# Optimization experiments

Measured on AMD Instinct MI355X. Metric: run time of the kernel, lower is better.

## Reference

```python
import jax, jax.numpy as jnp
import numpy as np

B, L, D_IN, H, TAGS = 16, 128, 512, 256, 45


def setup_inputs() -> dict:
    key = jax.random.key(0)
    ks = jax.random.split(key, 10)
    s = 0.02
    return {
        "contextualized": jax.random.normal(ks[0], (B, L, D_IN), jnp.float32),
        "sentence_lengths": jax.random.randint(ks[1], (B,), 64, L + 1, jnp.int32),
        "desired_arcs": jax.random.randint(ks[2], (B, L), 0, L + 1, jnp.int32),
        "desired_labels": jax.random.randint(ks[3], (B, L), 0, TAGS, jnp.int32),
        "W1": jax.random.normal(ks[4], (D_IN, H), jnp.float32) * s,
        "b1": jnp.zeros((H,), jnp.float32),
        "root": jax.random.normal(ks[5], (H,), jnp.float32) * s,
        "Wp": jax.random.normal(ks[6], (2 * H, H), jnp.float32) * s,
        "bp": jnp.zeros((H,), jnp.float32),
        "W_arc": jax.random.normal(ks[7], (H, 1), jnp.float32) * s,
        "b_arc": jnp.zeros((1,), jnp.float32),
        "W_lab": jax.random.normal(ks[8], (H, TAGS), jnp.float32) * s,
        "b_lab": jnp.zeros((TAGS,), jnp.float32),
    }


def _forward(contextualized, sentence_lengths, desired_arcs, desired_labels,
             W1, b1, root, Wp, bp, W_arc, b_arc, W_lab, b_lab):
    b, l, _ = contextualized.shape
    h = W1.shape[1]
    # token representations: dense + relu
    hidden = jax.nn.relu(contextualized @ W1 + b1)                      # [B,L,H]
    # prepend learned root vector
    root_t = jnp.broadcast_to(root, (b, 1, h))
    cwr = jnp.concatenate([root_t, hidden], axis=1)                     # [B,L+1,H]
    # pairs dense: concat([tile_a, tile_b]) @ Wp == hidden@Wa + cwr@Wb (broadcast-add)
    Wa, Wb = Wp[:h], Wp[h:]
    pre = (hidden @ Wa)[:, :, None, :] + (cwr @ Wb)[:, None, :, :] + bp
    pairs_repr = jax.nn.relu(pre)                                       # [B,L,L+1,H]
    # valid-token mask from sentence lengths
    mask = (jnp.arange(l)[None, :] < sentence_lengths[:, None]).astype(jnp.float32)
    denom = jnp.maximum(mask.sum(), 1.0)
    # UAS: arc logits over L+1 head candidates, softmax CE vs gold arcs
    arc_logits = jnp.squeeze(pairs_repr @ W_arc, -1) + b_arc[0]         # [B,L,L+1]
    arc_logp = jax.nn.log_softmax(arc_logits, axis=-1)
    arc_ce = -jnp.take_along_axis(arc_logp, desired_arcs[:, :, None], axis=-1)[..., 0]
    uas_loss = jnp.sum(arc_ce * mask) / denom
    # LAS: select pair repr at gold arc, dense -> tag logits, softmax CE
    sel = jnp.take_along_axis(pairs_repr, desired_arcs[:, :, None, None].astype(jnp.int32)
                              .repeat(1, axis=2), axis=2)[:, :, 0, :]   # [B,L,H]
    label_logits = sel @ W_lab + b_lab                                  # [B,L,TAGS]
    lab_logp = jax.nn.log_softmax(label_logits, axis=-1)
    lab_ce = -jnp.take_along_axis(lab_logp, desired_labels[:, :, None], axis=-1)[..., 0]
    las_loss = jnp.sum(lab_ce * mask) / denom
    return (uas_loss + las_loss) * 0.5


def reference(contextualized, sentence_lengths, desired_arcs, desired_labels,
              W1, b1, root, Wp, bp, W_arc, b_arc, W_lab, b_lab):
    return _forward(contextualized, sentence_lengths, desired_arcs, desired_labels,
                    W1, b1, root, Wp, bp, W_arc, b_arc, W_lab, b_lab)
```

## Files before the change

### kernel.cpp

```cpp
#include <hip/hip_runtime.h>
#include <math.h>

#define NB 16
#define NL 128
#define DIN 512
#define NH 256
#define NTAGS 45
#define NM (NB*NL)
#define NJ (NL+1)

#define H_OFF     0
#define U_OFF     (4*NM*NH)
#define HV_OFF    (6*NM*NH)
#define VROOT_OFF (8*NM*NH)
#define ACC_OFF   (VROOT_OFF + NH)

__global__ __launch_bounds__(256) void gemm_hidden(
    const float* __restrict__ A,
    const float* __restrict__ W,
    float* __restrict__ h,
    float* __restrict__ accum)
{
    __shared__ float As[16][68];
    __shared__ float Bs[16][68];
    int m0 = blockIdx.x * 64;
    int n0 = blockIdx.y * 64;
    int kbase = blockIdx.z * 128;
    int tid = threadIdx.x;
    if (blockIdx.x == 0 && blockIdx.y == 0 && blockIdx.z == 0 && tid == 0) {
        accum[0] = 0.f;
        ((int*)accum)[1] = 0;
    }
    int lm = tid >> 2, lk = (tid & 3) * 4;
    int bk = tid >> 4, bn = (tid & 15) * 4;
    int tm = tid >> 4, tn = tid & 15;
    float acc[4][4] = {{0.f}};

    for (int k0 = kbase; k0 < kbase + 128; k0 += 16) {
        float4 a4 = *(const float4*)&A[(size_t)(m0 + lm) * DIN + k0 + lk];
        As[lk + 0][lm] = a4.x; As[lk + 1][lm] = a4.y;
        As[lk + 2][lm] = a4.z; As[lk + 3][lm] = a4.w;
        float4 b4 = *(const float4*)&W[(size_t)(k0 + bk) * NH + n0 + bn];
        *(float4*)&Bs[bk][bn] = b4;
        __syncthreads();
        #pragma unroll
        for (int kk = 0; kk < 16; kk++) {
            float4 av = *(const float4*)&As[kk][tm * 4];
            float4 bv = *(const float4*)&Bs[kk][tn * 4];
            float ar[4] = {av.x, av.y, av.z, av.w};
            float br[4] = {bv.x, bv.y, bv.z, bv.w};
            #pragma unroll
            for (int r = 0; r < 4; r++)
                #pragma unroll
                for (int c = 0; c < 4; c++)
                    acc[r][c] = fmaf(ar[r], br[c], acc[r][c]);
        }
        __syncthreads();
    }
    float* hz = h + (size_t)blockIdx.z * NM * NH;
    int col = n0 + tn * 4;
    #pragma unroll
    for (int r = 0; r < 4; r++) {
        int row = m0 + tm * 4 + r;
        *(float4*)&hz[(size_t)row * NH + col] =
            make_float4(acc[r][0], acc[r][1], acc[r][2], acc[r][3]);
    }
}

__global__ __launch_bounds__(256) void gemm_uv(
    const float* __restrict__ h,
    const float* __restrict__ b1,
    const float* __restrict__ Wp,
    const float* __restrict__ root,
    float* __restrict__ uu,
    float* __restrict__ hvv,
    float* __restrict__ vroot)
{
    __shared__ float As[16][68];
    __shared__ float Bs[16][68];
    __shared__ float part[4][64];
    int n0 = blockIdx.y * 64;
    int tid = threadIdx.x;

    if (blockIdx.x == 32) {
        if (blockIdx.z != 0 || n0 < NH) return;
        int col = (n0 - NH) + (tid & 63);
        int kc = tid >> 6;
        float p = 0.f;
        #pragma unroll 8
        for (int c = kc * 64; c < kc * 64 + 64; c++)
            p += root[c] * Wp[(size_t)(NH + c) * NH + col];
        part[kc][tid & 63] = p;
        __syncthreads();
        if (tid < 64)
            vroot[(n0 - NH) + tid] = part[0][tid] + part[1][tid]
                                   + part[2][tid] + part[3][tid];
        return;
    }

    int m0 = blockIdx.x * 64;
    int kbase = blockIdx.z * 128;
    bool isU = (n0 < NH);
    int lm = tid >> 2, lk = (tid & 3) * 4;
    int bk = tid >> 4, bn = (tid & 15) * 4;
    int tm = tid >> 4, tn = tid & 15;
    float acc[4][4] = {{0.f}};

    for (int k0 = kbase; k0 < kbase + 128; k0 += 16) {
        size_t base = (size_t)(m0 + lm) * NH + k0 + lk;
        float4 p0 = *(const float4*)&h[base];
        float4 p1 = *(const float4*)&h[base + (size_t)1 * NM * NH];
        float4 p2 = *(const float4*)&h[base + (size_t)2 * NM * NH];
        float4 p3 = *(const float4*)&h[base + (size_t)3 * NM * NH];
        float4 bv = *(const float4*)&b1[k0 + lk];
        As[lk + 0][lm] = fmaxf(p0.x + p1.x + p2.x + p3.x + bv.x, 0.f);
        As[lk + 1][lm] = fmaxf(p0.y + p1.y + p2.y + p3.y + bv.y, 0.f);
        As[lk + 2][lm] = fmaxf(p0.z + p1.z + p2.z + p3.z + bv.z, 0.f);
        As[lk + 3][lm] = fmaxf(p0.w + p1.w + p2.w + p3.w + bv.w, 0.f);
        int c = k0 + bk;
        float4 b4;
        if (isU) b4 = *(const float4*)&Wp[(size_t)c * NH + n0 + bn];
        else     b4 = *(const float4*)&Wp[(size_t)(NH + c) * NH + (n0 - NH) + bn];
        *(float4*)&Bs[bk][bn] = b4;
        __syncthreads();
        #pragma unroll
        for (int kk = 0; kk < 16; kk++) {
            float4 av = *(const float4*)&As[kk][tm * 4];
            float4 bv2 = *(const float4*)&Bs[kk][tn * 4];
            float ar[4] = {av.x, av.y, av.z, av.w};
            float br[4] = {bv2.x, bv2.y, bv2.z, bv2.w};
            #pragma unroll
            for (int r = 0; r < 4; r++)
                #pragma unroll
                for (int cc = 0; cc < 4; cc++)
                    acc[r][cc] = fmaf(ar[r], br[cc], acc[r][cc]);
        }
        __syncthreads();
    }
    float* dst = (isU ? uu : hvv) + (size_t)blockIdx.z * NM * NH;
    int col = (isU ? n0 : n0 - NH) + tn * 4;
    #pragma unroll
    for (int r = 0; r < 4; r++) {
        int row = m0 + tm * 4 + r;
        *(float4*)&dst[(size_t)row * NH + col] =
            make_float4(acc[r][0], acc[r][1], acc[r][2], acc[r][3]);
    }
}

#define NBLK (NB*32)

__global__ __launch_bounds__(256) void score_loss_kernel(
    const float* __restrict__ uu, const float* __restrict__ hvv,
    const float* __restrict__ vroot, const float* __restrict__ W_arc,
    const float* __restrict__ bp,
    const float* __restrict__ W_lab, const float* __restrict__ b_lab,
    const int* __restrict__ slens, const int* __restrict__ arcs,
    const int* __restrict__ labels,
    float* __restrict__ accum, float* __restrict__ out)
{
    __shared__ float2 v2_s[32][129];
    __shared__ float2 u2_s[4][128];
    __shared__ float2 wa2_s[128];
    __shared__ float2 sel2_s[32][5];
    __shared__ float  ce_s[4];
    __shared__ int    arc_s[4], lab_s[4];

    int bb = blockIdx.x;
    int i0 = blockIdx.y * 4;
    int tid = threadIdx.x;
    int w = tid >> 6;
    int lane = tid & 63;
    int slen = slens[bb];

    if (i0 < slen) {
        {
            int r = tid >> 6, kq = (tid & 63) * 4;
            size_t base = (size_t)(bb * NL + i0 + r) * NH + kq;
            float4 a0 = *(const float4*)&uu[base];
            float4 a1 = *(const float4*)&uu[base + (size_t)NM * NH];
            float4 b4 = *(const float4*)&bp[kq];
            float4 a4 = make_float4(a0.x + a1.x + b4.x, a0.y + a1.y + b4.y,
                                    a0.z + a1.z + b4.z, a0.w + a1.w + b4.w);
            u2_s[r][(kq >> 1) + 0] = make_float2(a4.x, a4.y);
            u2_s[r][(kq >> 1) + 1] = make_float2(a4.z, a4.w);
        }
        if (tid < 128)
            wa2_s[tid] = *(const float2*)&W_arc[tid * 2];
        if (tid < 4) {
            int rg = bb * NL + i0 + tid;
            arc_s[tid] = arcs[rg];
            lab_s[tid] = labels[rg];
        }

        float acc1 = 0.f, acc2 = 0.f, s128 = 0.f, lacc = 0.f;

        for (int c = 0; c < 4; ++c) {
            int k0 = c * 64;
            for (int idx = tid; idx < NJ * 16; idx += 256) {
                int j = idx >> 4, kq = (idx & 15) * 4;
                float4 t4;
                if (j == 0) {
                    t4 = *(const float4*)&vroot[k0 + kq];
                } else {
                    size_t base = (size_t)(bb * NL + j - 1) * NH + k0 + kq;
                    float4 q0 = *(const float4*)&hvv[base];
                    float4 q1 = *(const float4*)&hvv[base + (size_t)NM * NH];
                    t4 = make_float4(q0.x + q1.x, q0.y + q1.y,
                                     q0.z + q1.z, q0.w + q1.w);
                }
                v2_s[(kq >> 1) + 0][j] = make_float2(t4.x, t4.y);
                v2_s[(kq >> 1) + 1][j] = make_float2(t4.z, t4.w);
            }
            __syncthreads();

            const float2* urow = u2_s[w] + (k0 >> 1);
            const float2* warow = wa2_s + (k0 >> 1);
            #pragma unroll 8
            for (int kk2 = 0; kk2 < 32; ++kk2) {
                float2 u2 = urow[kk2];
                float2 w2 = warow[kk2];
                float2 va = v2_s[kk2][lane];
                float2 vb = v2_s[kk2][lane + 64];
                acc1 += fmaxf(u2.x + va.x, 0.f) * w2.x
                      + fmaxf(u2.y + va.y, 0.f) * w2.y;
                acc2 += fmaxf(u2.x + vb.x, 0.f) * w2.x
                      + fmaxf(u2.y + vb.y, 0.f) * w2.y;
            }
            if (lane < 32) {
                float2 u2 = urow[lane];
                float2 w2 = warow[lane];
                float2 vv = v2_s[lane][128];
                s128 += fmaxf(u2.x + vv.x, 0.f) * w2.x
                      + fmaxf(u2.y + vv.y, 0.f) * w2.y;
                float2 vs = v2_s[lane][arc_s[w]];
                sel2_s[lane][w] = make_float2(fmaxf(u2.x + vs.x, 0.f),
                                              fmaxf(u2.y + vs.y, 0.f));
            }
            if (lane < NTAGS) {
                #pragma unroll 8
                for (int kk2 = 0; kk2 < 32; ++kk2) {
                    float2 s2 = sel2_s[kk2][w];
                    float w0 = W_lab[(size_t)(k0 + 2 * kk2) * NTAGS + lane];
                    float w1 = W_lab[(size_t)(k0 + 2 * kk2 + 1) * NTAGS + lane];
                    lacc = fmaf(s2.x, w0, fmaf(s2.y, w1, lacc));
                }
            }
            __syncthreads();
        }

        float s128t = s128;
        #pragma unroll
        for (int off = 32; off > 0; off >>= 1)
            s128t += __shfl_xor(s128t, off);
        float m = fmaxf(acc1, acc2);
        #pragma unroll
        for (int off = 32; off > 0; off >>= 1)
            m = fmaxf(m, __shfl_xor(m, off));
        m = fmaxf(m, s128t);
        float e = expf(acc1 - m) + expf(acc2 - m);
        #pragma unroll
        for (int off = 32; off > 0; off >>= 1)
            e += __shfl_xor(e, off);
        e += expf(s128t - m);
        int a = arc_s[w];
        float cand = (a < 64) ? acc1 : acc2;
        float s_a = __shfl(cand, a & 63, 64);
        if (a == 128) s_a = s128t;
        float arc_ce = (m + logf(e)) - s_a;

        float logit = (lane < NTAGS) ? (lacc + b_lab[lane]) : -INFINITY;
        float m2 = logit;
        #pragma unroll
        for (int off = 32; off > 0; off >>= 1)
            m2 = fmaxf(m2, __shfl_xor(m2, off));
        float e2 = (lane < NTAGS) ? expf(logit - m2) : 0.f;
        #pragma unroll
        for (int off = 32; off > 0; off >>= 1)
            e2 += __shfl_xor(e2, off);
        float l_t = __shfl(logit, lab_s[w], 64);
        float lab_ce = (m2 + logf(e2)) - l_t;

        float tot = ((i0 + w) < slen) ? (arc_ce + lab_ce) : 0.f;
        if (lane == 0) ce_s[w] = tot;
        __syncthreads();
        if (tid == 0)
            atomicAdd(accum, ce_s[0] + ce_s[1] + ce_s[2] + ce_s[3]);
    }

    if (tid == 0) {
        __threadfence();
        int prev = atomicAdd((int*)accum + 1, 1);
        if (prev == NBLK - 1) {
            int d = 0;
            #pragma unroll
            for (int q = 0; q < NB; ++q) d += slens[q];
            float s = atomicAdd(accum, 0.f);
            out[0] = 0.5f * s / fmaxf((float)d, 1.f);
        }
    }
}

extern "C" void kernel_launch(void* const* d_in, const int* in_sizes, int n_in,
                              void* d_out, int out_size, void* d_ws, size_t ws_size,
                              hipStream_t stream) {
    (void)in_sizes; (void)n_in; (void)out_size; (void)ws_size;
    const float* ctx   = (const float*)d_in[0];
    const int*   slens = (const int*)  d_in[1];
    const int*   arcs  = (const int*)  d_in[2];
    const int*   labs  = (const int*)  d_in[3];
    const float* W1    = (const float*)d_in[4];
    const float* b1    = (const float*)d_in[5];
    const float* root  = (const float*)d_in[6];
    const float* Wp    = (const float*)d_in[7];
    const float* bp    = (const float*)d_in[8];
    const float* W_arc = (const float*)d_in[9];
    const float* W_lab = (const float*)d_in[11];
    const float* b_lab = (const float*)d_in[12];
    float* out = (float*)d_out;

    float* ws    = (float*)d_ws;
    float* h     = ws + H_OFF;
    float* u     = ws + U_OFF;
    float* hv    = ws + HV_OFF;
    float* vroot = ws + VROOT_OFF;
    float* accum = ws + ACC_OFF;

    gemm_hidden<<<dim3(32, 4, 4), 256, 0, stream>>>(ctx, W1, h, accum);
    gemm_uv<<<dim3(33, 8, 2), 256, 0, stream>>>(h, b1, Wp, root, u, hv, vroot);
    score_loss_kernel<<<dim3(NB, 32), 256, 0, stream>>>(
        u, hv, vroot, W_arc, bp, W_lab, b_lab, slens, arcs, labs, accum, out);
}
```

Measured before the change: 151.1 us.

## Split arc-score kernel over head halves with two-pass log-sum-exp merge

The score/loss kernel gets a third grid dimension that splits the 129 head candidates into two halves, so each block stages and scores only about 65 columns. Each half writes partial max/sum-exp values to workspace, the half that owns the gold arc writes the selected score and label CE, and the last block merges them with a numerically stable combine. This doubles the number of blocks to fill more CUs and shrinks LDS use per block, at the cost of extra global writes and a serial final reduction in one block. Both GEMM kernels also move from a K-tile of 16 to 32, halving the number of barrier pairs per K slice.

```diff
diff --git a/kernel.cpp b/kernel.cpp
--- a/kernel.cpp
+++ b/kernel.cpp
@@ -14,6 +14,10 @@
 #define HV_OFF    (6*NM*NH)
 #define VROOT_OFF (8*NM*NH)
 #define ACC_OFF   (VROOT_OFF + NH)
+#define PM_OFF    (ACC_OFF + 4)
+#define PE_OFF    (PM_OFF + 2*NM)
+#define SA_OFF    (PE_OFF + 2*NM)
+#define LCE_OFF   (SA_OFF + NM)
 
 __global__ __launch_bounds__(256) void gemm_hidden(
     const float* __restrict__ A,
@@ -21,8 +25,8 @@
     float* __restrict__ h,
     float* __restrict__ accum)
 {
-    __shared__ float As[16][68];
-    __shared__ float Bs[16][68];
+    __shared__ float As[32][68];
+    __shared__ float Bs[32][68];
     int m0 = blockIdx.x * 64;
     int n0 = blockIdx.y * 64;
     int kbase = blockIdx.z * 128;
@@ -31,20 +35,24 @@
         accum[0] = 0.f;
         ((int*)accum)[1] = 0;
     }
-    int lm = tid >> 2, lk = (tid & 3) * 4;
-    int bk = tid >> 4, bn = (tid & 15) * 4;
     int tm = tid >> 4, tn = tid & 15;
     float acc[4][4] = {{0.f}};
 
-    for (int k0 = kbase; k0 < kbase + 128; k0 += 16) {
-        float4 a4 = *(const float4*)&A[(size_t)(m0 + lm) * DIN + k0 + lk];
-        As[lk + 0][lm] = a4.x; As[lk + 1][lm] = a4.y;
-        As[lk + 2][lm] = a4.z; As[lk + 3][lm] = a4.w;
-        float4 b4 = *(const float4*)&W[(size_t)(k0 + bk) * NH + n0 + bn];
-        *(float4*)&Bs[bk][bn] = b4;
-        __syncthreads();
-        #pragma unroll
-        for (int kk = 0; kk < 16; kk++) {
+    for (int k0 = kbase; k0 < kbase + 128; k0 += 32) {
+        #pragma unroll
+        for (int s = 0; s < 2; s++) {
+            int idx = tid + s * 256;
+            int arow = idx >> 3, akq = (idx & 7) * 4;
+            float4 a4 = *(const float4*)&A[(size_t)(m0 + arow) * DIN + k0 + akq];
+            As[akq + 0][arow] = a4.x; As[akq + 1][arow] = a4.y;
+            As[akq + 2][arow] = a4.z; As[akq + 3][arow] = a4.w;
+            int bk = idx >> 4, bn = (idx & 15) * 4;
+            *(float4*)&Bs[bk][bn] =
+                *(const float4*)&W[(size_t)(k0 + bk) * NH + n0 + bn];
+        }
+        __syncthreads();
+        #pragma unroll
+        for (int kk = 0; kk < 32; kk++) {
             float4 av = *(const float4*)&As[kk][tm * 4];
             float4 bv = *(const float4*)&Bs[kk][tn * 4];
             float ar[4] = {av.x, av.y, av.z, av.w};
@@ -76,8 +84,8 @@
     float* __restrict__ hvv,
     float* __restrict__ vroot)
 {
-    __shared__ float As[16][68];
-    __shared__ float Bs[16][68];
+    __shared__ float As[32][68];
+    __shared__ float Bs[32][68];
     __shared__ float part[4][64];
     int n0 = blockIdx.y * 64;
     int tid = threadIdx.x;
@@ -101,30 +109,34 @@
     int m0 = blockIdx.x * 64;
     int kbase = blockIdx.z * 128;
     bool isU = (n0 < NH);
-    int lm = tid >> 2, lk = (tid & 3) * 4;
-    int bk = tid >> 4, bn = (tid & 15) * 4;
     int tm = tid >> 4, tn = tid & 15;
     float acc[4][4] = {{0.f}};
 
-    for (int k0 = kbase; k0 < kbase + 128; k0 += 16) {
-        size_t base = (size_t)(m0 + lm) * NH + k0 + lk;
-        float4 p0 = *(const float4*)&h[base];
-        float4 p1 = *(const float4*)&h[base + (size_t)1 * NM * NH];
-        float4 p2 = *(const float4*)&h[base + (size_t)2 * NM * NH];
-        float4 p3 = *(const float4*)&h[base + (size_t)3 * NM * NH];
-        float4 bv = *(const float4*)&b1[k0 + lk];
-        As[lk + 0][lm] = fmaxf(p0.x + p1.x + p2.x + p3.x + bv.x, 0.f);
-        As[lk + 1][lm] = fmaxf(p0.y + p1.y + p2.y + p3.y + bv.y, 0.f);
-        As[lk + 2][lm] = fmaxf(p0.z + p1.z + p2.z + p3.z + bv.z, 0.f);
-        As[lk + 3][lm] = fmaxf(p0.w + p1.w + p2.w + p3.w + bv.w, 0.f);
-        int c = k0 + bk;
-        float4 b4;
-        if (isU) b4 = *(const float4*)&Wp[(size_t)c * NH + n0 + bn];
-        else     b4 = *(const float4*)&Wp[(size_t)(NH + c) * NH + (n0 - NH) + bn];
-        *(float4*)&Bs[bk][bn] = b4;
-        __syncthreads();
-        #pragma unroll
-        for (int kk = 0; kk < 16; kk++) {
+    for (int k0 = kbase; k0 < kbase + 128; k0 += 32) {
+        #pragma unroll
+        for (int s = 0; s < 2; s++) {
+            int idx = tid + s * 256;
+            int arow = idx >> 3, akq = (idx & 7) * 4;
+            size_t base = (size_t)(m0 + arow) * NH + k0 + akq;
+            float4 p0 = *(const float4*)&h[base];
+            float4 p1 = *(const float4*)&h[base + (size_t)1 * NM * NH];
+            float4 p2 = *(const float4*)&h[base + (size_t)2 * NM * NH];
+            float4 p3 = *(const float4*)&h[base + (size_t)3 * NM * NH];
+            float4 bv = *(const float4*)&b1[k0 + akq];
+            As[akq + 0][arow] = fmaxf(p0.x + p1.x + p2.x + p3.x + bv.x, 0.f);
+            As[akq + 1][arow] = fmaxf(p0.y + p1.y + p2.y + p3.y + bv.y, 0.f);
+            As[akq + 2][arow] = fmaxf(p0.z + p1.z + p2.z + p3.z + bv.z, 0.f);
+            As[akq + 3][arow] = fmaxf(p0.w + p1.w + p2.w + p3.w + bv.w, 0.f);
+            int bk = idx >> 4, bn = (idx & 15) * 4;
+            int c = k0 + bk;
+            float4 b4;
+            if (isU) b4 = *(const float4*)&Wp[(size_t)c * NH + n0 + bn];
+            else     b4 = *(const float4*)&Wp[(size_t)(NH + c) * NH + (n0 - NH) + bn];
+            *(float4*)&Bs[bk][bn] = b4;
+        }
+        __syncthreads();
+        #pragma unroll
+        for (int kk = 0; kk < 32; kk++) {
             float4 av = *(const float4*)&As[kk][tm * 4];
             float4 bv2 = *(const float4*)&Bs[kk][tn * 4];
             float ar[4] = {av.x, av.y, av.z, av.w};
@@ -147,7 +159,7 @@
     }
 }
 
-#define NBLK (NB*32)
+#define NBLK (NB*32*2)
 
 __global__ __launch_bounds__(256) void score_loss_kernel(
     const float* __restrict__ uu, const float* __restrict__ hvv,
@@ -156,21 +168,27 @@
     const float* __restrict__ W_lab, const float* __restrict__ b_lab,
     const int* __restrict__ slens, const int* __restrict__ arcs,
     const int* __restrict__ labels,
+    float* __restrict__ pm, float* __restrict__ pe,
+    float* __restrict__ sa, float* __restrict__ lce,
     float* __restrict__ accum, float* __restrict__ out)
 {
-    __shared__ float2 v2_s[32][129];
+    __shared__ float2 v2_s[32][66];
     __shared__ float2 u2_s[4][128];
     __shared__ float2 wa2_s[128];
     __shared__ float2 sel2_s[32][5];
-    __shared__ float  ce_s[4];
+    __shared__ float  rs_s[4];
     __shared__ int    arc_s[4], lab_s[4];
+    __shared__ int    lastf;
 
     int bb = blockIdx.x;
     int i0 = blockIdx.y * 4;
+    int h  = blockIdx.z;
     int tid = threadIdx.x;
     int w = tid >> 6;
     int lane = tid & 63;
     int slen = slens[bb];
+    const int j0 = h ? 64 : 0;
+    const int njh = 64 + h;
 
     if (i0 < slen) {
         {
@@ -179,10 +197,10 @@
             float4 a0 = *(const float4*)&uu[base];
             float4 a1 = *(const float4*)&uu[base + (size_t)NM * NH];
             float4 b4 = *(const float4*)&bp[kq];
-            float4 a4 = make_float4(a0.x + a1.x + b4.x, a0.y + a1.y + b4.y,
-                                    a0.z + a1.z + b4.z, a0.w + a1.w + b4.w);
-            u2_s[r][(kq >> 1) + 0] = make_float2(a4.x, a4.y);
-            u2_s[r][(kq >> 1) + 1] = make_float2(a4.z, a4.w);
+            u2_s[r][(kq >> 1) + 0] = make_float2(a0.x + a1.x + b4.x,
+                                                 a0.y + a1.y + b4.y);
+            u2_s[r][(kq >> 1) + 1] = make_float2(a0.z + a1.z + b4.z,
+                                                 a0.w + a1.w + b4.w);
         }
         if (tid < 128)
             wa2_s[tid] = *(const float2*)&W_arc[tid * 2];
@@ -192,26 +210,30 @@
             lab_s[tid] = labels[rg];
         }
 
-        float acc1 = 0.f, acc2 = 0.f, s128 = 0.f, lacc = 0.f;
+        float acc = 0.f, s128 = 0.f, lacc = 0.f;
 
         for (int c = 0; c < 4; ++c) {
             int k0 = c * 64;
-            for (int idx = tid; idx < NJ * 16; idx += 256) {
-                int j = idx >> 4, kq = (idx & 15) * 4;
+            for (int idx = tid; idx < njh * 16; idx += 256) {
+                int jl = idx >> 4, kq = (idx & 15) * 4;
+                int jg = j0 + jl;
                 float4 t4;
-                if (j == 0) {
+                if (jg == 0) {
                     t4 = *(const float4*)&vroot[k0 + kq];
                 } else {
-                    size_t base = (size_t)(bb * NL + j - 1) * NH + k0 + kq;
+                    size_t base = (size_t)(bb * NL + jg - 1) * NH + k0 + kq;
                     float4 q0 = *(const float4*)&hvv[base];
                     float4 q1 = *(const float4*)&hvv[base + (size_t)NM * NH];
                     t4 = make_float4(q0.x + q1.x, q0.y + q1.y,
                                      q0.z + q1.z, q0.w + q1.w);
                 }
-                v2_s[(kq >> 1) + 0][j] = make_float2(t4.x, t4.y);
-                v2_s[(kq >> 1) + 1][j] = make_float2(t4.z, t4.w);
+                v2_s[(kq >> 1) + 0][jl] = make_float2(t4.x, t4.y);
+                v2_s[(kq >> 1) + 1][jl] = make_float2(t4.z, t4.w);
             }
             __syncthreads();
+
+            int a = arc_s[w];
+            bool own = (a >= j0) && (a - j0 < njh);
 
             const float2* urow = u2_s[w] + (k0 >> 1);
             const float2* warow = wa2_s + (k0 >> 1);
@@ -220,29 +242,31 @@
                 float2 u2 = urow[kk2];
                 float2 w2 = warow[kk2];
                 float2 va = v2_s[kk2][lane];
-                float2 vb = v2_s[kk2][lane + 64];
-                acc1 += fmaxf(u2.x + va.x, 0.f) * w2.x
-                      + fmaxf(u2.y + va.y, 0.f) * w2.y;
-                acc2 += fmaxf(u2.x + vb.x, 0.f) * w2.x
-                      + fmaxf(u2.y + vb.y, 0.f) * w2.y;
-            }
-            if (lane < 32) {
+                acc += fmaxf(u2.x + va.x, 0.f) * w2.x
+                     + fmaxf(u2.y + va.y, 0.f) * w2.y;
+            }
+            if (h && lane < 32) {
                 float2 u2 = urow[lane];
                 float2 w2 = warow[lane];
-                float2 vv = v2_s[lane][128];
+                float2 vv = v2_s[lane][64];
                 s128 += fmaxf(u2.x + vv.x, 0.f) * w2.x
                       + fmaxf(u2.y + vv.y, 0.f) * w2.y;
-                float2 vs = v2_s[lane][arc_s[w]];
-                sel2_s[lane][w] = make_float2(fmaxf(u2.x + vs.x, 0.f),
-                                              fmaxf(u2.y + vs.y, 0.f));
-            }
-            if (lane < NTAGS) {
-                #pragma unroll 8
-                for (int kk2 = 0; kk2 < 32; ++kk2) {
-                    float2 s2 = sel2_s[kk2][w];
-                    float w0 = W_lab[(size_t)(k0 + 2 * kk2) * NTAGS + lane];
-                    float w1 = W_lab[(size_t)(k0 + 2 * kk2 + 1) * NTAGS + lane];
-                    lacc = fmaf(s2.x, w0, fmaf(s2.y, w1, lacc));
+            }
+            if (own) {
+                if (lane < 32) {
+                    float2 u2 = urow[lane];
+                    float2 vs = v2_s[lane][a - j0];
+                    sel2_s[lane][w] = make_float2(fmaxf(u2.x + vs.x, 0.f),
+                                                  fmaxf(u2.y + vs.y, 0.f));
+                }
+                if (lane < NTAGS) {
+                    #pragma unroll 8
+                    for (int kk2 = 0; kk2 < 32; ++kk2) {
+                        float2 s2 = sel2_s[kk2][w];
+                        float w0 = W_lab[(size_t)(k0 + 2 * kk2) * NTAGS + lane];
+                        float w1 = W_lab[(size_t)(k0 + 2 * kk2 + 1) * NTAGS + lane];
+                        lacc = fmaf(s2.x, w0, fmaf(s2.y, w1, lacc));
+                    }
                 }
             }
             __syncthreads();
@@ -252,50 +276,71 @@
         #pragma unroll
         for (int off = 32; off > 0; off >>= 1)
             s128t += __shfl_xor(s128t, off);
-        float m = fmaxf(acc1, acc2);
+        float m = acc;
         #pragma unroll
         for (int off = 32; off > 0; off >>= 1)
             m = fmaxf(m, __shfl_xor(m, off));
-        m = fmaxf(m, s128t);
-        float e = expf(acc1 - m) + expf(acc2 - m);
+        if (h) m = fmaxf(m, s128t);
+        float e = expf(acc - m);
         #pragma unroll
         for (int off = 32; off > 0; off >>= 1)
             e += __shfl_xor(e, off);
-        e += expf(s128t - m);
+        if (h) e += expf(s128t - m);
+        int row = bb * NL + i0 + w;
+        if (lane == 0) {
+            pm[h * NM + row] = m;
+            pe[h * NM + row] = e;
+        }
+
         int a = arc_s[w];
-        float cand = (a < 64) ? acc1 : acc2;
-        float s_a = __shfl(cand, a & 63, 64);
-        if (a == 128) s_a = s128t;
-        float arc_ce = (m + logf(e)) - s_a;
-
-        float logit = (lane < NTAGS) ? (lacc + b_lab[lane]) : -INFINITY;
-        float m2 = logit;
+        if ((a >= j0) && (a - j0 < njh)) {
+            float s_a = (a - j0 < 64) ? __shfl(acc, a - j0, 64) : s128t;
+            float logit = (lane < NTAGS) ? (lacc + b_lab[lane]) : -INFINITY;
+            float m2 = logit;
+            #pragma unroll
+            for (int off = 32; off > 0; off >>= 1)
+                m2 = fmaxf(m2, __shfl_xor(m2, off));
+            float e2 = (lane < NTAGS) ? expf(logit - m2) : 0.f;
+            #pragma unroll
+            for (int off = 32; off > 0; off >>= 1)
+                e2 += __shfl_xor(e2, off);
+            float lt = __shfl(logit, lab_s[w], 64);
+            if (lane == 0) {
+                sa[row] = s_a;
+                lce[row] = (m2 + logf(e2)) - lt;
+            }
+        }
+    }
+
+    __threadfence();
+    __syncthreads();
+    if (tid == 0)
+        lastf = (atomicAdd((int*)accum + 1, 1) == NBLK - 1);
+    __syncthreads();
+    if (lastf) {
+        __threadfence();
+        float sum = 0.f;
+        for (int r = tid; r < NM; r += 256) {
+            int b = r >> 7, i = r & 127;
+            if (i < slens[b]) {
+                float m0 = pm[r], m1 = pm[NM + r];
+                float e0 = pe[r], e1 = pe[NM + r];
+                float M = fmaxf(m0, m1);
+                float E = e0 * expf(m0 - M) + e1 * expf(m1 - M);
+                sum += (M + logf(E)) - sa[r] + lce[r];
+            }
+        }
         #pragma unroll
         for (int off = 32; off > 0; off >>= 1)
-            m2 = fmaxf(m2, __shfl_xor(m2, off));
-        float e2 = (lane < NTAGS) ? expf(logit - m2) : 0.f;
-        #pragma unroll
-        for (int off = 32; off > 0; off >>= 1)
-            e2 += __shfl_xor(e2, off);
-        float l_t = __shfl(logit, lab_s[w], 64);
-        float lab_ce = (m2 + logf(e2)) - l_t;
-
-        float tot = ((i0 + w) < slen) ? (arc_ce + lab_ce) : 0.f;
-        if (lane == 0) ce_s[w] = tot;
-        __syncthreads();
-        if (tid == 0)
-            atomicAdd(accum, ce_s[0] + ce_s[1] + ce_s[2] + ce_s[3]);
-    }
-
-    if (tid == 0) {
-        __threadfence();
-        int prev = atomicAdd((int*)accum + 1, 1);
-        if (prev == NBLK - 1) {
+            sum += __shfl_xor(sum, off);
+        if (lane == 0) rs_s[tid >> 6] = sum;
+        __syncthreads();
+        if (tid == 0) {
             int d = 0;
             #pragma unroll
             for (int q = 0; q < NB; ++q) d += slens[q];
-            float s = atomicAdd(accum, 0.f);
-            out[0] = 0.5f * s / fmaxf((float)d, 1.f);
+            out[0] = 0.5f * (rs_s[0] + rs_s[1] + rs_s[2] + rs_s[3])
+                   / fmaxf((float)d, 1.f);
         }
     }
 }
@@ -324,9 +369,14 @@
     float* hv    = ws + HV_OFF;
     float* vroot = ws + VROOT_OFF;
     float* accum = ws + ACC_OFF;
+    float* pm    = ws + PM_OFF;
+    float* pe    = ws + PE_OFF;
+    float* sal   = ws + SA_OFF;
+    float* lcel  = ws + LCE_OFF;
 
     gemm_hidden<<<dim3(32, 4, 4), 256, 0, stream>>>(ctx, W1, h, accum);
     gemm_uv<<<dim3(33, 8, 2), 256, 0, stream>>>(h, b1, Wp, root, u, hv, vroot);
-    score_loss_kernel<<<dim3(NB, 32), 256, 0, stream>>>(
-        u, hv, vroot, W_arc, bp, W_lab, b_lab, slens, arcs, labs, accum, out);
+    score_loss_kernel<<<dim3(NB, 32, 2), 256, 0, stream>>>(
+        u, hv, vroot, W_arc, bp, W_lab, b_lab, slens, arcs, labs,
+        pm, pe, sal, lcel, accum, out);
 }
```

Measured after the change: 215.0 us. 1.42x slower.

## Double-buffer GEMM and score tiles, reduce split-K, fold bias into u

Applied to the files above, without the earlier changes.

Both GEMM kernels now keep a register-prefetched, double-buffered shared tile so the global loads for the next k-chunk overlap the FMA loop. The score kernel prefetches the next v chunk the same way. Split-K drops from 4 to 2 for the hidden GEMM and is removed for the uv GEMM, which cuts partial-sum traffic and the extra reductions downstream, and the bp bias is added in the GEMM epilogue. In exchange there are fewer blocks in flight, more shared memory per block, and nine float4 prefetch registers per thread in the score kernel.

```diff
diff --git a/kernel.cpp b/kernel.cpp
--- a/kernel.cpp
+++ b/kernel.cpp
@@ -10,9 +10,9 @@
 #define NJ (NL+1)
 
 #define H_OFF     0
-#define U_OFF     (4*NM*NH)
-#define HV_OFF    (6*NM*NH)
-#define VROOT_OFF (8*NM*NH)
+#define U_OFF     (2*NM*NH)
+#define HV_OFF    (3*NM*NH)
+#define VROOT_OFF (4*NM*NH)
 #define ACC_OFF   (VROOT_OFF + NH)
 
 __global__ __launch_bounds__(256) void gemm_hidden(
@@ -21,41 +21,56 @@
     float* __restrict__ h,
     float* __restrict__ accum)
 {
-    __shared__ float As[16][68];
-    __shared__ float Bs[16][68];
+    __shared__ float As[2][16][68];
+    __shared__ float Bs[2][16][68];
     int m0 = blockIdx.x * 64;
     int n0 = blockIdx.y * 64;
-    int kbase = blockIdx.z * 128;
+    int kbase = blockIdx.z * 256;
     int tid = threadIdx.x;
     if (blockIdx.x == 0 && blockIdx.y == 0 && blockIdx.z == 0 && tid == 0) {
         accum[0] = 0.f;
         ((int*)accum)[1] = 0;
     }
-    int lm = tid >> 2, lk = (tid & 3) * 4;
+    int arow = tid >> 2, akq = (tid & 3) * 4;
     int bk = tid >> 4, bn = (tid & 15) * 4;
     int tm = tid >> 4, tn = tid & 15;
     float acc[4][4] = {{0.f}};
-
-    for (int k0 = kbase; k0 < kbase + 128; k0 += 16) {
-        float4 a4 = *(const float4*)&A[(size_t)(m0 + lm) * DIN + k0 + lk];
-        As[lk + 0][lm] = a4.x; As[lk + 1][lm] = a4.y;
-        As[lk + 2][lm] = a4.z; As[lk + 3][lm] = a4.w;
-        float4 b4 = *(const float4*)&W[(size_t)(k0 + bk) * NH + n0 + bn];
-        *(float4*)&Bs[bk][bn] = b4;
-        __syncthreads();
+    float4 a_r, b_r;
+
+    auto LOADK = [&](int c) {
+        int k0 = kbase + c * 16;
+        a_r = *(const float4*)&A[(size_t)(m0 + arow) * DIN + k0 + akq];
+        b_r = *(const float4*)&W[(size_t)(k0 + bk) * NH + n0 + bn];
+    };
+    auto WRITE = [&](int buf) {
+        As[buf][akq + 0][arow] = a_r.x; As[buf][akq + 1][arow] = a_r.y;
+        As[buf][akq + 2][arow] = a_r.z; As[buf][akq + 3][arow] = a_r.w;
+        *(float4*)&Bs[buf][bk][bn] = b_r;
+    };
+
+    LOADK(0);
+    WRITE(0);
+    LOADK(1);
+    __syncthreads();
+    for (int c = 0; c < 16; ++c) {
+        int buf = c & 1;
         #pragma unroll
         for (int kk = 0; kk < 16; kk++) {
-            float4 av = *(const float4*)&As[kk][tm * 4];
-            float4 bv = *(const float4*)&Bs[kk][tn * 4];
+            float4 av = *(const float4*)&As[buf][kk][tm * 4];
+            float4 bv = *(const float4*)&Bs[buf][kk][tn * 4];
             float ar[4] = {av.x, av.y, av.z, av.w};
             float br[4] = {bv.x, bv.y, bv.z, bv.w};
             #pragma unroll
             for (int r = 0; r < 4; r++)
                 #pragma unroll
-                for (int c = 0; c < 4; c++)
-                    acc[r][c] = fmaf(ar[r], br[c], acc[r][c]);
-        }
-        __syncthreads();
+                for (int cc = 0; cc < 4; cc++)
+                    acc[r][cc] = fmaf(ar[r], br[cc], acc[r][cc]);
+        }
+        if (c < 15) {
+            WRITE(buf ^ 1);
+            if (c < 14) LOADK(c + 2);
+            __syncthreads();
+        }
     }
     float* hz = h + (size_t)blockIdx.z * NM * NH;
     int col = n0 + tn * 4;
@@ -71,19 +86,20 @@
     const float* __restrict__ h,
     const float* __restrict__ b1,
     const float* __restrict__ Wp,
+    const float* __restrict__ bp,
     const float* __restrict__ root,
-    float* __restrict__ uu,
-    float* __restrict__ hvv,
+    float* __restrict__ u,
+    float* __restrict__ hv,
     float* __restrict__ vroot)
 {
-    __shared__ float As[16][68];
-    __shared__ float Bs[16][68];
+    __shared__ float As[2][16][68];
+    __shared__ float Bs[2][16][68];
     __shared__ float part[4][64];
     int n0 = blockIdx.y * 64;
     int tid = threadIdx.x;
 
     if (blockIdx.x == 32) {
-        if (blockIdx.z != 0 || n0 < NH) return;
+        if (n0 < NH) return;
         int col = (n0 - NH) + (tid & 63);
         int kc = tid >> 6;
         float p = 0.f;
@@ -99,60 +115,81 @@
     }
 
     int m0 = blockIdx.x * 64;
-    int kbase = blockIdx.z * 128;
     bool isU = (n0 < NH);
-    int lm = tid >> 2, lk = (tid & 3) * 4;
+    int arow = tid >> 2, akq = (tid & 3) * 4;
     int bk = tid >> 4, bn = (tid & 15) * 4;
     int tm = tid >> 4, tn = tid & 15;
     float acc[4][4] = {{0.f}};
-
-    for (int k0 = kbase; k0 < kbase + 128; k0 += 16) {
-        size_t base = (size_t)(m0 + lm) * NH + k0 + lk;
-        float4 p0 = *(const float4*)&h[base];
-        float4 p1 = *(const float4*)&h[base + (size_t)1 * NM * NH];
-        float4 p2 = *(const float4*)&h[base + (size_t)2 * NM * NH];
-        float4 p3 = *(const float4*)&h[base + (size_t)3 * NM * NH];
-        float4 bv = *(const float4*)&b1[k0 + lk];
-        As[lk + 0][lm] = fmaxf(p0.x + p1.x + p2.x + p3.x + bv.x, 0.f);
-        As[lk + 1][lm] = fmaxf(p0.y + p1.y + p2.y + p3.y + bv.y, 0.f);
-        As[lk + 2][lm] = fmaxf(p0.z + p1.z + p2.z + p3.z + bv.z, 0.f);
-        As[lk + 3][lm] = fmaxf(p0.w + p1.w + p2.w + p3.w + bv.w, 0.f);
-        int c = k0 + bk;
-        float4 b4;
-        if (isU) b4 = *(const float4*)&Wp[(size_t)c * NH + n0 + bn];
-        else     b4 = *(const float4*)&Wp[(size_t)(NH + c) * NH + (n0 - NH) + bn];
-        *(float4*)&Bs[bk][bn] = b4;
-        __syncthreads();
+    float4 ha_r, hb_r, bi_r, b_r;
+
+    auto LOADK = [&](int c) {
+        int k0 = c * 16;
+        size_t base = (size_t)(m0 + arow) * NH + k0 + akq;
+        ha_r = *(const float4*)&h[base];
+        hb_r = *(const float4*)&h[base + (size_t)NM * NH];
+        bi_r = *(const float4*)&b1[k0 + akq];
+        int ck = k0 + bk;
+        if (isU) b_r = *(const float4*)&Wp[(size_t)ck * NH + n0 + bn];
+        else     b_r = *(const float4*)&Wp[(size_t)(NH + ck) * NH + (n0 - NH) + bn];
+    };
+    auto WRITE = [&](int buf) {
+        As[buf][akq + 0][arow] = fmaxf(ha_r.x + hb_r.x + bi_r.x, 0.f);
+        As[buf][akq + 1][arow] = fmaxf(ha_r.y + hb_r.y + bi_r.y, 0.f);
+        As[buf][akq + 2][arow] = fmaxf(ha_r.z + hb_r.z + bi_r.z, 0.f);
+        As[buf][akq + 3][arow] = fmaxf(ha_r.w + hb_r.w + bi_r.w, 0.f);
+        *(float4*)&Bs[buf][bk][bn] = b_r;
+    };
+
+    LOADK(0);
+    WRITE(0);
+    LOADK(1);
+    __syncthreads();
+    for (int c = 0; c < 16; ++c) {
+        int buf = c & 1;
         #pragma unroll
         for (int kk = 0; kk < 16; kk++) {
-            float4 av = *(const float4*)&As[kk][tm * 4];
-            float4 bv2 = *(const float4*)&Bs[kk][tn * 4];
+            float4 av = *(const float4*)&As[buf][kk][tm * 4];
+            float4 bv = *(const float4*)&Bs[buf][kk][tn * 4];
             float ar[4] = {av.x, av.y, av.z, av.w};
-            float br[4] = {bv2.x, bv2.y, bv2.z, bv2.w};
+            float br[4] = {bv.x, bv.y, bv.z, bv.w};
             #pragma unroll
             for (int r = 0; r < 4; r++)
                 #pragma unroll
                 for (int cc = 0; cc < 4; cc++)
                     acc[r][cc] = fmaf(ar[r], br[cc], acc[r][cc]);
         }
-        __syncthreads();
-    }
-    float* dst = (isU ? uu : hvv) + (size_t)blockIdx.z * NM * NH;
-    int col = (isU ? n0 : n0 - NH) + tn * 4;
-    #pragma unroll
-    for (int r = 0; r < 4; r++) {
-        int row = m0 + tm * 4 + r;
-        *(float4*)&dst[(size_t)row * NH + col] =
-            make_float4(acc[r][0], acc[r][1], acc[r][2], acc[r][3]);
+        if (c < 15) {
+            WRITE(buf ^ 1);
+            if (c < 14) LOADK(c + 2);
+            __syncthreads();
+        }
+    }
+    if (isU) {
+        int col = n0 + tn * 4;
+        float4 bb = *(const float4*)&bp[col];
+        #pragma unroll
+        for (int r = 0; r < 4; r++) {
+            int row = m0 + tm * 4 + r;
+            *(float4*)&u[(size_t)row * NH + col] = make_float4(
+                acc[r][0] + bb.x, acc[r][1] + bb.y,
+                acc[r][2] + bb.z, acc[r][3] + bb.w);
+        }
+    } else {
+        int col = (n0 - NH) + tn * 4;
+        #pragma unroll
+        for (int r = 0; r < 4; r++) {
+            int row = m0 + tm * 4 + r;
+            *(float4*)&hv[(size_t)row * NH + col] = make_float4(
+                acc[r][0], acc[r][1], acc[r][2], acc[r][3]);
+        }
     }
 }
 
 #define NBLK (NB*32)
 
 __global__ __launch_bounds__(256) void score_loss_kernel(
-    const float* __restrict__ uu, const float* __restrict__ hvv,
+    const float* __restrict__ u, const float* __restrict__ hv,
     const float* __restrict__ vroot, const float* __restrict__ W_arc,
-    const float* __restrict__ bp,
     const float* __restrict__ W_lab, const float* __restrict__ b_lab,
     const int* __restrict__ slens, const int* __restrict__ arcs,
     const int* __restrict__ labels,
@@ -175,12 +212,7 @@
     if (i0 < slen) {
         {
             int r = tid >> 6, kq = (tid & 63) * 4;
-            size_t base = (size_t)(bb * NL + i0 + r) * NH + kq;
-            float4 a0 = *(const float4*)&uu[base];
-            float4 a1 = *(const float4*)&uu[base + (size_t)NM * NH];
-            float4 b4 = *(const float4*)&bp[kq];
-            float4 a4 = make_float4(a0.x + a1.x + b4.x, a0.y + a1.y + b4.y,
-                                    a0.z + a1.z + b4.z, a0.w + a1.w + b4.w);
+            float4 a4 = *(const float4*)&u[(size_t)(bb * NL + i0 + r) * NH + kq];
             u2_s[r][(kq >> 1) + 0] = make_float2(a4.x, a4.y);
             u2_s[r][(kq >> 1) + 1] = make_float2(a4.z, a4.w);
         }
@@ -192,26 +224,41 @@
             lab_s[tid] = labels[rg];
         }
 
+        float4 vr[9];
+        auto VLOAD = [&](int c) {
+            int k0 = c * 64;
+            #pragma unroll
+            for (int s = 0; s < 9; ++s) {
+                int idx = tid + s * 256;
+                if (idx < NJ * 16) {
+                    int j = idx >> 4, kq = (idx & 15) * 4;
+                    const float* src = (j == 0) ? (vroot + k0 + kq)
+                        : (hv + (size_t)(bb * NL + j - 1) * NH + k0 + kq);
+                    vr[s] = *(const float4*)src;
+                }
+            }
+        };
+        auto VWRITE = [&]() {
+            #pragma unroll
+            for (int s = 0; s < 9; ++s) {
+                int idx = tid + s * 256;
+                if (idx < NJ * 16) {
+                    int j = idx >> 4, kq = (idx & 15) * 4;
+                    v2_s[(kq >> 1) + 0][j] = make_float2(vr[s].x, vr[s].y);
+                    v2_s[(kq >> 1) + 1][j] = make_float2(vr[s].z, vr[s].w);
+                }
+            }
+        };
+
         float acc1 = 0.f, acc2 = 0.f, s128 = 0.f, lacc = 0.f;
 
+        VLOAD(0);
         for (int c = 0; c < 4; ++c) {
+            if (c) __syncthreads();
+            VWRITE();
+            __syncthreads();
+            if (c < 3) VLOAD(c + 1);
             int k0 = c * 64;
-            for (int idx = tid; idx < NJ * 16; idx += 256) {
-                int j = idx >> 4, kq = (idx & 15) * 4;
-                float4 t4;
-                if (j == 0) {
-                    t4 = *(const float4*)&vroot[k0 + kq];
-                } else {
-                    size_t base = (size_t)(bb * NL + j - 1) * NH + k0 + kq;
-                    float4 q0 = *(const float4*)&hvv[base];
-                    float4 q1 = *(const float4*)&hvv[base + (size_t)NM * NH];
-                    t4 = make_float4(q0.x + q1.x, q0.y + q1.y,
-                                     q0.z + q1.z, q0.w + q1.w);
-                }
-                v2_s[(kq >> 1) + 0][j] = make_float2(t4.x, t4.y);
-                v2_s[(kq >> 1) + 1][j] = make_float2(t4.z, t4.w);
-            }
-            __syncthreads();
 
             const float2* urow = u2_s[w] + (k0 >> 1);
             const float2* warow = wa2_s + (k0 >> 1);
@@ -245,7 +292,6 @@
                     lacc = fmaf(s2.x, w0, fmaf(s2.y, w1, lacc));
                 }
             }
-            __syncthreads();
         }
 
         float s128t = s128;
@@ -325,8 +371,8 @@
     float* vroot = ws + VROOT_OFF;
     float* accum = ws + ACC_OFF;
 
-    gemm_hidden<<<dim3(32, 4, 4), 256, 0, stream>>>(ctx, W1, h, accum);
-    gemm_uv<<<dim3(33, 8, 2), 256, 0, stream>>>(h, b1, Wp, root, u, hv, vroot);
+    gemm_hidden<<<dim3(32, 4, 2), 256, 0, stream>>>(ctx, W1, h, accum);
+    gemm_uv<<<dim3(33, 8), 256, 0, stream>>>(h, b1, Wp, bp, root, u, hv, vroot);
     score_loss_kernel<<<dim3(NB, 32), 256, 0, stream>>>(
-        u, hv, vroot, W_arc, bp, W_lab, b_lab, slens, arcs, labs, accum, out);
+        u, hv, vroot, W_arc, W_lab, b_lab, slens, arcs, labs, accum, out);
 }
```

New measurement: 139.7 us. 1.08x faster.
